# Performance work log

Measured on AMD Instinct MI355X. Metric: run time of the kernel, lower is better.

## Reference

```python
import jax, jax.numpy as jnp
import numpy as np

EPS = 1e-5
GROUPS = 8
OUT_PLANES = 256
GP = OUT_PLANES // GROUPS  # group_planes = 32


def _bn_eval(x, p, ch_axis):
    # p: [4, C] = (gamma, beta, running_mean, running_var); eval-mode batchnorm
    shape = [1] * x.ndim
    shape[ch_axis] = -1
    g, b, m, v = (p[i].reshape(shape) for i in range(4))
    return g * (x - m) * jax.lax.rsqrt(v + EPS) + b


def _make_bn(key, ch):
    k1, k2, k3, k4 = jax.random.split(key, 4)
    gamma = jax.random.uniform(k1, (ch,)) + 0.5
    beta = jax.random.normal(k2, (ch,)) * 0.1
    mean = jax.random.normal(k3, (ch,)) * 0.1
    var = jax.random.uniform(k4, (ch,)) + 0.5
    return jnp.stack([gamma, beta, mean, var])  # [4, ch]


def setup_inputs() -> dict:
    key = jax.random.key(0)
    ks = jax.random.split(key, 6)
    N, C, D, Hh, Ww = 1, 256, 16, 32, 64
    x = jax.random.normal(ks[0], (N, C, D, Hh, Ww), dtype=jnp.float32)
    # qkv 1x1 conv weight: [out_planes*2, in_planes]
    qkv_w = jax.random.normal(ks[1], (OUT_PLANES * 2, C), dtype=jnp.float32) * np.sqrt(1.0 / C)
    # relative positional table: [group_planes*2, 2*H-1]
    relative = jax.random.normal(ks[2], (GP * 2, 2 * Ww - 1), dtype=jnp.float32) * np.sqrt(1.0 / GP)
    bn_qkv = _make_bn(ks[3], OUT_PLANES * 2)
    bn_sim = _make_bn(ks[4], GROUPS * 3)
    bn_out = _make_bn(ks[5], OUT_PLANES * 2)
    return {"x": x, "qkv_w": qkv_w, "relative": relative,
            "bn_qkv": bn_qkv, "bn_sim": bn_sim, "bn_out": bn_out}


def reference(x, qkv_w, relative, bn_qkv, bn_sim, bn_out):
    N, C, D, Hh, Ww = x.shape
    G, OP, gp = GROUPS, OUT_PLANES, GP
    # width == 0: permute(0,2,3,1,4) -> [N, D, Hh, C, Ww]; attend along Ww
    xp = jnp.transpose(x, (0, 2, 3, 1, 4))
    H = Ww
    B = N * D * Hh
    xr = xp.reshape(B, C, H)
    # 1x1 conv + BN over channels
    qkv = jnp.einsum('oc,bch->boh', qkv_w, xr)
    qkv = _bn_eval(qkv, bn_qkv, 1)
    qkv = qkv.reshape(B, G, 2 * gp, H)
    q = qkv[:, :, : gp // 2]          # [B,G,gp/2,H]
    k = qkv[:, :, gp // 2: gp]        # [B,G,gp/2,H]
    v = qkv[:, :, gp:]                # [B,G,gp,H]
    # relative-position gather: emb[c,i,j] = relative[c, i-j+H-1]
    idx = jnp.arange(H)[:, None] - jnp.arange(H)[None, :] + H - 1  # [H,H]
    emb = relative[:, idx]            # [2*gp, H, H]
    q_e = emb[: gp // 2]
    k_e = emb[gp // 2: gp]
    v_e = emb[gp:]
    qr = jnp.einsum('bgci,cij->bgij', q, q_e)
    kr = jnp.einsum('bgci,cij->bgji', k, k_e)  # einsum + transpose(2,3) fused
    qk = jnp.einsum('bgci,bgcj->bgij', q, k)
    sim = jnp.concatenate([qk, qr, kr], axis=1)  # [B, 3G, H, H]
    sim = _bn_eval(sim, bn_sim, 1)
    sim = sim.reshape(B, 3, G, H, H).sum(axis=1)
    sim = jax.nn.softmax(sim, axis=3)
    sv = jnp.einsum('bgij,bgcj->bgci', sim, v)
    sve = jnp.einsum('bgij,cij->bgci', sim, v_e)
    so = jnp.concatenate([sv, sve], axis=-1).reshape(B, 2 * OP, H)
    out = _bn_eval(so, bn_out, 1)
    out = out.reshape(N, D, Hh, OP, 2, H).sum(axis=-2)
    out = jnp.transpose(out, (0, 3, 1, 2, 4))  # [N, OP, D, Hh, Ww]
    return out
```

## Files before the change

### kernel.cpp

```cpp
#include <hip/hip_runtime.h>

#define EPS 1e-5f

typedef _Float16 half4_t __attribute__((ext_vector_type(4)));
typedef _Float16 half8_t __attribute__((ext_vector_type(8)));
typedef float floatx4 __attribute__((ext_vector_type(4)));

__device__ __forceinline__ unsigned short f2hb(float f) {
  _Float16 h = (_Float16)f;
  return __builtin_bit_cast(unsigned short, h);
}
__device__ __forceinline__ float hb2f(unsigned short u) {
  return (float)__builtin_bit_cast(_Float16, u);
}
__device__ __forceinline__ unsigned int pack2(float a, float b) {
  return (unsigned int)f2hb(a) | ((unsigned int)f2hb(b) << 16);
}

#define WS_QKT 16777216
#define WS_WH 33554432
#define WS_RELTQ 33816576
#define WS_RELTK 33820672
#define WS_RELV 33824768
#define WS_BNSF 33832960
#define WS_BNOSC 33833088
#define WS_BNOSH 33835136

__global__ __launch_bounds__(256) void k_prep(const float* __restrict__ W,
                                              const float* __restrict__ rel,
                                              const float* __restrict__ bns,
                                              const float* __restrict__ bno,
                                              char* __restrict__ ws) {
  const int bid = blockIdx.x, tid = threadIdx.x;
  if (bid < 8) {
    unsigned short* Wh = (unsigned short*)(ws + WS_WH);
    const int base = bid * 16384;
#pragma unroll
    for (int u = 0; u < 16; ++u) {
      const int i = base + u * 1024 + tid * 4;
      const float4 v = *reinterpret_cast<const float4*>(&W[i]);
      uint2 p;
      p.x = pack2(v.x, v.y);
      p.y = pack2(v.z, v.w);
      *reinterpret_cast<uint2*>(&Wh[i]) = p;
    }
  } else {
    unsigned short* relTq = (unsigned short*)(ws + WS_RELTQ);
    unsigned short* relTk = (unsigned short*)(ws + WS_RELTK);
    unsigned short* relV = (unsigned short*)(ws + WS_RELV);
    float* bnsF = (float*)(ws + WS_BNSF);
    float* bnoSc = (float*)(ws + WS_BNOSC);
    float* bnoSh = (float*)(ws + WS_BNOSH);
    for (int idx = tid; idx < 2048; idx += 256) {
      const int t = idx >> 4, c = idx & 15;
      relTq[idx] = (t < 127) ? f2hb(rel[c * 127 + t]) : (unsigned short)0;
      relTk[idx] = (t < 127) ? f2hb(rel[(16 + c) * 127 + t]) : (unsigned short)0;
    }
    for (int idx = tid; idx < 4096; idx += 256) {
      const int c = idx >> 7, t = idx & 127;
      relV[idx] = (t < 127) ? f2hb(rel[(32 + c) * 127 + t]) : (unsigned short)0;
    }
    if (tid < 8) {
      const int g = tid;
      const float scA = bns[g] / sqrtf(bns[72 + g] + EPS);
      const float scB = bns[8 + g] / sqrtf(bns[72 + 8 + g] + EPS);
      const float scC = bns[16 + g] / sqrtf(bns[72 + 16 + g] + EPS);
      const float shv = (bns[24 + g] - bns[48 + g] * scA) +
                        (bns[24 + 8 + g] - bns[48 + 8 + g] * scB) +
                        (bns[24 + 16 + g] - bns[48 + 16 + g] * scC);
      bnsF[g * 4 + 0] = scA;
      bnsF[g * 4 + 1] = scB;
      bnsF[g * 4 + 2] = scC;
      bnsF[g * 4 + 3] = shv;
    }
    for (int idx = tid; idx < 512; idx += 256) {
      const float sc = bno[idx] / sqrtf(bno[1536 + idx] + EPS);
      bnoSc[idx] = sc;
      bnoSh[idx] = bno[512 + idx] - bno[1024 + idx] * sc;
    }
  }
}

__global__ __launch_bounds__(512, 4) void k_qkv(const float* __restrict__ x,
                                                const float* __restrict__ bnq,
                                                char* __restrict__ ws) {
  const unsigned short* Wh = (const unsigned short*)(ws + WS_WH);
  unsigned short* qkv_h = (unsigned short*)ws;
  unsigned short* qkT = (unsigned short*)(ws + WS_QKT);
  __shared__ __align__(16) char arena[67584];
  unsigned short* xT = (unsigned short*)arena;
  unsigned short* qk_t = (unsigned short*)arena;
  unsigned short* v_t = (unsigned short*)(arena + 33792);

  const int tid = threadIdx.x;
  const int lane = tid & 63;
  const int w = tid >> 6;
  const int l15 = lane & 15, kg = lane >> 4;
  const size_t b = blockIdx.x;
  const int n0g = (int)b * 64;

  {
    const int k = tid >> 1;
    const int nb = (tid & 1) * 32;
    const float* src = x + (size_t)k * 32768 + n0g + nb;
    unsigned short hv[32];
#pragma unroll
    for (int u = 0; u < 8; ++u) {
      const float4 v4 = *reinterpret_cast<const float4*>(src + u * 4);
      hv[u * 4 + 0] = f2hb(v4.x);
      hv[u * 4 + 1] = f2hb(v4.y);
      hv[u * 4 + 2] = f2hb(v4.z);
      hv[u * 4 + 3] = f2hb(v4.w);
    }
#pragma unroll
    for (int e = 0; e < 32; ++e) xT[(nb + e) * 280 + k] = hv[e];
  }
  __syncthreads();

  floatx4 acc[4][4] = {};
#pragma unroll
  for (int kk = 0; kk < 8; ++kk) {
    half8_t af[4], bf[4];
#pragma unroll
    for (int fm = 0; fm < 4; ++fm)
      af[fm] = *reinterpret_cast<const half8_t*>(Wh + (size_t)(w * 64 + fm * 16 + l15) * 256 +
                                                 kk * 32 + kg * 8);
#pragma unroll
    for (int fn = 0; fn < 4; ++fn)
      bf[fn] =
          *reinterpret_cast<const half8_t*>(xT + (fn * 16 + l15) * 280 + kk * 32 + kg * 8);
#pragma unroll
    for (int fm = 0; fm < 4; ++fm)
#pragma unroll
      for (int fn = 0; fn < 4; ++fn)
        acc[fm][fn] = __builtin_amdgcn_mfma_f32_16x16x32_f16(af[fm], bf[fn], acc[fm][fn], 0, 0, 0);
  }
  __syncthreads();

  const int o0 = w * 64;
#pragma unroll
  for (int fm = 0; fm < 4; ++fm) {
    float sc[4], sh[4];
#pragma unroll
    for (int reg = 0; reg < 4; ++reg) {
      const int o = o0 + fm * 16 + kg * 4 + reg;
      sc[reg] = bnq[o] / sqrtf(bnq[1536 + o] + EPS);
      sh[reg] = bnq[512 + o] - bnq[1024 + o] * sc[reg];
    }
#pragma unroll
    for (int fn = 0; fn < 4; ++fn) {
      const int h = fn * 16 + l15;
#pragma unroll
      for (int reg = 0; reg < 4; ++reg) {
        const int row = fm * 16 + kg * 4 + reg;
        const float val = fmaf(acc[fm][fn][reg], sc[reg], sh[reg]);
        if (fm < 2) {
          qk_t[w * 2112 + h * 33 + row] = f2hb(val);
        } else {
          v_t[w * 2112 + (row - 32) * 66 + h] = f2hb(val);
        }
      }
    }
  }
  __syncthreads();

  {
    const int half = tid >> 8;
    const int tt = tid & 255;
#pragma unroll
    for (int it = 0; it < 4; ++it) {
      const int g = it * 2 + half;
      {
        const int h = tt >> 2, c0 = (tt & 3) * 8;
        unsigned short tmp[8];
#pragma unroll
        for (int e = 0; e < 8; ++e) tmp[e] = qk_t[g * 2112 + h * 33 + c0 + e];
        uint4 wv;
        wv.x = (unsigned int)tmp[0] | ((unsigned int)tmp[1] << 16);
        wv.y = (unsigned int)tmp[2] | ((unsigned int)tmp[3] << 16);
        wv.z = (unsigned int)tmp[4] | ((unsigned int)tmp[5] << 16);
        wv.w = (unsigned int)tmp[6] | ((unsigned int)tmp[7] << 16);
        *reinterpret_cast<uint4*>(&qkT[((b * 8 + g) * 64 + h) * 32 + c0]) = wv;
      }
      {
        const int c = tt >> 3, h0 = (tt & 7) * 8;
        unsigned short tmp[8];
#pragma unroll
        for (int e = 0; e < 8; ++e) tmp[e] = v_t[g * 2112 + c * 66 + h0 + e];
        uint4 wv;
        wv.x = (unsigned int)tmp[0] | ((unsigned int)tmp[1] << 16);
        wv.y = (unsigned int)tmp[2] | ((unsigned int)tmp[3] << 16);
        wv.z = (unsigned int)tmp[4] | ((unsigned int)tmp[5] << 16);
        wv.w = (unsigned int)tmp[6] | ((unsigned int)tmp[7] << 16);
        *reinterpret_cast<uint4*>(&qkv_h[((b * 8 + g) * 32 + c) * 64 + h0]) = wv;
      }
    }
  }
}

#define QKS 36
#define M1S 132
#define PBS 72
#define PPS 136
#define OTS 67

__global__ __launch_bounds__(256, 4) void k_attn(const char* __restrict__ ws,
                                                 float* __restrict__ out) {
  const unsigned short* qkv_h = (const unsigned short*)ws;
  const unsigned short* qkTg = (const unsigned short*)(ws + WS_QKT);
  const unsigned short* relTq = (const unsigned short*)(ws + WS_RELTQ);
  const unsigned short* relTk = (const unsigned short*)(ws + WS_RELTK);
  const unsigned short* relV = (const unsigned short*)(ws + WS_RELV);
  const float* bnsF = (const float*)(ws + WS_BNSF);
  const float* bnoSc = (const float*)(ws + WS_BNOSC);
  const float* bnoSh = (const float*)(ws + WS_BNOSH);

  __shared__ __align__(16) char arena[38400];
  unsigned short* qkL = (unsigned short*)arena;
  unsigned short* M1 = (unsigned short*)(arena + 4608);
  unsigned short* M2 = (unsigned short*)(arena + 21504);
  unsigned short* Pb = (unsigned short*)arena;
  unsigned short* Pp = (unsigned short*)(arena + 9216);
  unsigned short* Vb = (unsigned short*)(arena + 26624);
  float* Sout = (float*)arena;

  const int tid = threadIdx.x;
  const int lane = tid & 63;
  const int wid = tid >> 6;
  const int l15 = lane & 15, kg = lane >> 4;
  const int bg = blockIdx.x;
  const int b = bg >> 3, g = bg & 7;

  {
    const uint4 qv =
        *reinterpret_cast<const uint4*>(&qkTg[(size_t)(((b << 3) + g)) * 2048 + tid * 8]);
    const int i = tid >> 2, c0 = (tid & 3) * 8;
    uint2 lo, hi;
    lo.x = qv.x; lo.y = qv.y; hi.x = qv.z; hi.y = qv.w;
    *reinterpret_cast<uint2*>(&qkL[i * QKS + c0]) = lo;
    *reinterpret_cast<uint2*>(&qkL[i * QKS + c0 + 4]) = hi;
  }
  __syncthreads();

  floatx4 qkreg[4];
  {
    half4_t brq[8], brk[8];
#pragma unroll
    for (int nt = 0; nt < 8; ++nt) {
      brq[nt] = *reinterpret_cast<const half4_t*>(&relTq[(nt * 16 + l15) * 16 + kg * 4]);
      brk[nt] = *reinterpret_cast<const half4_t*>(&relTk[(nt * 16 + l15) * 16 + kg * 4]);
    }
    const half4_t aq = *reinterpret_cast<const half4_t*>(&qkL[(wid * 16 + l15) * QKS + kg * 4]);
    const half4_t ak =
        *reinterpret_cast<const half4_t*>(&qkL[(wid * 16 + l15) * QKS + 16 + kg * 4]);
#pragma unroll
    for (int nt = 0; nt < 4; ++nt) {
      const half4_t bq =
          *reinterpret_cast<const half4_t*>(&qkL[(nt * 16 + l15) * QKS + 16 + kg * 4]);
      const floatx4 z = {};
      qkreg[nt] = __builtin_amdgcn_mfma_f32_16x16x16f16(aq, bq, z, 0, 0, 0);
    }
#pragma unroll
    for (int nt = 0; nt < 8; ++nt) {
      const floatx4 z = {};
      const floatx4 cr = __builtin_amdgcn_mfma_f32_16x16x16f16(aq, brq[nt], z, 0, 0, 0);
#pragma unroll
      for (int r = 0; r < 4; ++r)
        M1[(wid * 16 + kg * 4 + r) * M1S + nt * 16 + l15] = f2hb(cr[r]);
    }
#pragma unroll
    for (int nt = 0; nt < 8; ++nt) {
      const floatx4 z = {};
      const floatx4 cr = __builtin_amdgcn_mfma_f32_16x16x16f16(ak, brk[nt], z, 0, 0, 0);
#pragma unroll
      for (int r = 0; r < 4; ++r)
        M2[(wid * 16 + kg * 4 + r) * M1S + nt * 16 + l15] = f2hb(cr[r]);
    }
  }
  __syncthreads();

  const uint4 vld = *reinterpret_cast<const uint4*>(
      &qkv_h[(((size_t)b * 8 + g) * 32 + (tid >> 3)) * 64 + (tid & 7) * 8]);
  float sreg[4][4];
  {
    const float4 bf = *reinterpret_cast<const float4*>(&bnsF[g * 4]);
#pragma unroll
    for (int nt = 0; nt < 4; ++nt) {
      const int j = nt * 16 + l15;
#pragma unroll
      for (int r = 0; r < 4; ++r) {
        const int i = wid * 16 + kg * 4 + r;
        const int d = i - j + 63;
        const float qr = hb2f(M1[i * M1S + d]);
        const float kr = hb2f(M2[j * M1S + 126 - d]);
        sreg[nt][r] = fmaf(bf.x, qkreg[nt][r], fmaf(bf.y, qr, fmaf(bf.z, kr, bf.w)));
      }
    }
  }
  __syncthreads();

  float sm[4];
#pragma unroll
  for (int r = 0; r < 4; ++r) {
    float m = fmaxf(fmaxf(sreg[0][r], sreg[1][r]), fmaxf(sreg[2][r], sreg[3][r]));
    m = fmaxf(m, __shfl_xor(m, 1));
    m = fmaxf(m, __shfl_xor(m, 2));
    m = fmaxf(m, __shfl_xor(m, 4));
    m = fmaxf(m, __shfl_xor(m, 8));
    float s = 0.f;
#pragma unroll
    for (int nt = 0; nt < 4; ++nt) {
      sreg[nt][r] = __expf(sreg[nt][r] - m);
      s += sreg[nt][r];
    }
    s += __shfl_xor(s, 1);
    s += __shfl_xor(s, 2);
    s += __shfl_xor(s, 4);
    s += __shfl_xor(s, 8);
    sm[r] = s;
  }
#pragma unroll
  for (int r = 0; r < 4; ++r) {
    const int i = wid * 16 + kg * 4 + r;
#pragma unroll
    for (int nt = 0; nt < 4; ++nt) {
      const int j = nt * 16 + l15;
      const unsigned short pv = f2hb(sreg[nt][r]);
      Pb[i * PBS + j] = pv;
      Pp[i * PPS + i + 63 - j] = pv;
    }
#pragma unroll
    for (int e = 0; e < 4; ++e) {
      const int z = l15 * 4 + e;
      const int t = (z < i) ? z : z + 64;
      Pp[i * PPS + t] = 0;
    }
  }
  {
    *reinterpret_cast<uint4*>(&Vb[(tid >> 3) * PBS + (tid & 7) * 8]) = vld;
  }
  __syncthreads();

  floatx4 sva[2] = {}, svea[2] = {};
#pragma unroll
  for (int kk = 0; kk < 2; ++kk) {
    const half8_t pa =
        *reinterpret_cast<const half8_t*>(&Pb[(wid * 16 + l15) * PBS + kk * 32 + kg * 8]);
#pragma unroll
    for (int nt = 0; nt < 2; ++nt) {
      const half8_t vb =
          *reinterpret_cast<const half8_t*>(&Vb[(nt * 16 + l15) * PBS + kk * 32 + kg * 8]);
      sva[nt] = __builtin_amdgcn_mfma_f32_16x16x32_f16(pa, vb, sva[nt], 0, 0, 0);
    }
  }
#pragma unroll
  for (int kk = 0; kk < 4; ++kk) {
    const half8_t pp =
        *reinterpret_cast<const half8_t*>(&Pp[(wid * 16 + l15) * PPS + kk * 32 + kg * 8]);
#pragma unroll
    for (int nt = 0; nt < 2; ++nt) {
      const half8_t rb =
          *reinterpret_cast<const half8_t*>(&relV[(nt * 16 + l15) * 128 + kk * 32 + kg * 8]);
      svea[nt] = __builtin_amdgcn_mfma_f32_16x16x32_f16(pp, rb, svea[nt], 0, 0, 0);
    }
  }
  __syncthreads();

#pragma unroll
  for (int nt = 0; nt < 2; ++nt) {
    const int c = nt * 16 + l15;
    const int ch = ((g << 5) + c) * 2;
    const float2 scv = *reinterpret_cast<const float2*>(&bnoSc[ch]);
    const float2 shv = *reinterpret_cast<const float2*>(&bnoSh[ch]);
#pragma unroll
    for (int r = 0; r < 4; ++r) {
      const int i = wid * 16 + kg * 4 + r;
      const float inv = 1.0f / sm[r];
      Sout[c * OTS + i] =
          fmaf(scv.x, sva[nt][r] * inv, shv.x) + fmaf(scv.y, svea[nt][r] * inv, shv.y);
    }
  }
  __syncthreads();
  {
    const size_t outbase = (size_t)b * 64;
#pragma unroll
    for (int r = 0; r < 8; ++r) {
      const int idx = tid + r * 256;
      const int cc = idx >> 6, ii = idx & 63;
      out[(size_t)((g << 5) + cc) * 32768 + outbase + ii] = Sout[cc * OTS + ii];
    }
  }
}

extern "C" void kernel_launch(void* const* d_in, const int* in_sizes, int n_in,
                              void* d_out, int out_size, void* d_ws, size_t ws_size,
                              hipStream_t stream) {
  const float* x = (const float*)d_in[0];
  const float* qkv_w = (const float*)d_in[1];
  const float* relative = (const float*)d_in[2];
  const float* bn_qkv = (const float*)d_in[3];
  const float* bn_sim = (const float*)d_in[4];
  const float* bn_out = (const float*)d_in[5];
  float* out = (float*)d_out;
  char* ws = (char*)d_ws;

  k_prep<<<9, 256, 0, stream>>>(qkv_w, relative, bn_sim, bn_out, ws);
  k_qkv<<<512, 512, 0, stream>>>(x, bn_qkv, ws);
  k_attn<<<4096, 256, 0, stream>>>(ws, out);
}
```

Baseline: 93.90 us.

## Restructure qkv/attn epilogues: precompute BN, direct V stores, transposed MFMA outputs

```diff
diff --git a/kernel.cpp b/kernel.cpp
--- a/kernel.cpp
+++ b/kernel.cpp
@@ -25,8 +25,11 @@
 #define WS_BNSF 33832960
 #define WS_BNOSC 33833088
 #define WS_BNOSH 33835136
+#define WS_BNQSC 33837184
+#define WS_BNQSH 33839232
 
 __global__ __launch_bounds__(256) void k_prep(const float* __restrict__ W,
+                                              const float* __restrict__ bnq,
                                               const float* __restrict__ rel,
                                               const float* __restrict__ bns,
                                               const float* __restrict__ bno,
@@ -51,6 +54,8 @@
     float* bnsF = (float*)(ws + WS_BNSF);
     float* bnoSc = (float*)(ws + WS_BNOSC);
     float* bnoSh = (float*)(ws + WS_BNOSH);
+    float* bnqSc = (float*)(ws + WS_BNQSC);
+    float* bnqSh = (float*)(ws + WS_BNQSH);
     for (int idx = tid; idx < 2048; idx += 256) {
       const int t = idx >> 4, c = idx & 15;
       relTq[idx] = (t < 127) ? f2hb(rel[c * 127 + t]) : (unsigned short)0;
@@ -77,20 +82,23 @@
       const float sc = bno[idx] / sqrtf(bno[1536 + idx] + EPS);
       bnoSc[idx] = sc;
       bnoSh[idx] = bno[512 + idx] - bno[1024 + idx] * sc;
-    }
-  }
-}
-
-__global__ __launch_bounds__(512, 4) void k_qkv(const float* __restrict__ x,
-                                                const float* __restrict__ bnq,
+      const float qc = bnq[idx] / sqrtf(bnq[1536 + idx] + EPS);
+      bnqSc[idx] = qc;
+      bnqSh[idx] = bnq[512 + idx] - bnq[1024 + idx] * qc;
+    }
+  }
+}
+
+__global__ __launch_bounds__(512, 8) void k_qkv(const float* __restrict__ x,
                                                 char* __restrict__ ws) {
   const unsigned short* Wh = (const unsigned short*)(ws + WS_WH);
+  const float* bnqSc = (const float*)(ws + WS_BNQSC);
+  const float* bnqSh = (const float*)(ws + WS_BNQSH);
   unsigned short* qkv_h = (unsigned short*)ws;
   unsigned short* qkT = (unsigned short*)(ws + WS_QKT);
-  __shared__ __align__(16) char arena[67584];
+  __shared__ __align__(16) char arena[36864];
   unsigned short* xT = (unsigned short*)arena;
   unsigned short* qk_t = (unsigned short*)arena;
-  unsigned short* v_t = (unsigned short*)(arena + 33792);
 
   const int tid = threadIdx.x;
   const int lane = tid & 63;
@@ -127,8 +135,7 @@
                                                  kk * 32 + kg * 8);
 #pragma unroll
     for (int fn = 0; fn < 4; ++fn)
-      bf[fn] =
-          *reinterpret_cast<const half8_t*>(xT + (fn * 16 + l15) * 280 + kk * 32 + kg * 8);
+      bf[fn] = *reinterpret_cast<const half8_t*>(xT + (fn * 16 + l15) * 280 + kk * 32 + kg * 8);
 #pragma unroll
     for (int fm = 0; fm < 4; ++fm)
 #pragma unroll
@@ -140,69 +147,52 @@
   const int o0 = w * 64;
 #pragma unroll
   for (int fm = 0; fm < 4; ++fm) {
-    float sc[4], sh[4];
-#pragma unroll
-    for (int reg = 0; reg < 4; ++reg) {
-      const int o = o0 + fm * 16 + kg * 4 + reg;
-      sc[reg] = bnq[o] / sqrtf(bnq[1536 + o] + EPS);
-      sh[reg] = bnq[512 + o] - bnq[1024 + o] * sc[reg];
-    }
+    const float4 sc4 = *reinterpret_cast<const float4*>(&bnqSc[o0 + fm * 16 + kg * 4]);
+    const float4 sh4 = *reinterpret_cast<const float4*>(&bnqSh[o0 + fm * 16 + kg * 4]);
 #pragma unroll
     for (int fn = 0; fn < 4; ++fn) {
       const int h = fn * 16 + l15;
-#pragma unroll
-      for (int reg = 0; reg < 4; ++reg) {
-        const int row = fm * 16 + kg * 4 + reg;
-        const float val = fmaf(acc[fm][fn][reg], sc[reg], sh[reg]);
-        if (fm < 2) {
-          qk_t[w * 2112 + h * 33 + row] = f2hb(val);
-        } else {
-          v_t[w * 2112 + (row - 32) * 66 + h] = f2hb(val);
-        }
+      const float v0 = fmaf(acc[fm][fn][0], sc4.x, sh4.x);
+      const float v1 = fmaf(acc[fm][fn][1], sc4.y, sh4.y);
+      const float v2 = fmaf(acc[fm][fn][2], sc4.z, sh4.z);
+      const float v3 = fmaf(acc[fm][fn][3], sc4.w, sh4.w);
+      if (fm < 2) {
+        uint2 p;
+        p.x = pack2(v0, v1);
+        p.y = pack2(v2, v3);
+        *reinterpret_cast<uint2*>(&qk_t[w * 2304 + h * 36 + fm * 16 + kg * 4]) = p;
+      } else {
+        const int cb = (fm - 2) * 16 + kg * 4;
+        unsigned short* dst = &qkv_h[((b * 8 + w) * 32 + cb) * 64 + h];
+        dst[0] = f2hb(v0);
+        dst[64] = f2hb(v1);
+        dst[128] = f2hb(v2);
+        dst[192] = f2hb(v3);
       }
     }
   }
   __syncthreads();
-
-  {
-    const int half = tid >> 8;
-    const int tt = tid & 255;
-#pragma unroll
-    for (int it = 0; it < 4; ++it) {
-      const int g = it * 2 + half;
-      {
-        const int h = tt >> 2, c0 = (tt & 3) * 8;
-        unsigned short tmp[8];
-#pragma unroll
-        for (int e = 0; e < 8; ++e) tmp[e] = qk_t[g * 2112 + h * 33 + c0 + e];
-        uint4 wv;
-        wv.x = (unsigned int)tmp[0] | ((unsigned int)tmp[1] << 16);
-        wv.y = (unsigned int)tmp[2] | ((unsigned int)tmp[3] << 16);
-        wv.z = (unsigned int)tmp[4] | ((unsigned int)tmp[5] << 16);
-        wv.w = (unsigned int)tmp[6] | ((unsigned int)tmp[7] << 16);
-        *reinterpret_cast<uint4*>(&qkT[((b * 8 + g) * 64 + h) * 32 + c0]) = wv;
-      }
-      {
-        const int c = tt >> 3, h0 = (tt & 7) * 8;
-        unsigned short tmp[8];
-#pragma unroll
-        for (int e = 0; e < 8; ++e) tmp[e] = v_t[g * 2112 + c * 66 + h0 + e];
-        uint4 wv;
-        wv.x = (unsigned int)tmp[0] | ((unsigned int)tmp[1] << 16);
-        wv.y = (unsigned int)tmp[2] | ((unsigned int)tmp[3] << 16);
-        wv.z = (unsigned int)tmp[4] | ((unsigned int)tmp[5] << 16);
-        wv.w = (unsigned int)tmp[6] | ((unsigned int)tmp[7] << 16);
-        *reinterpret_cast<uint4*>(&qkv_h[((b * 8 + g) * 32 + c) * 64 + h0]) = wv;
-      }
-    }
+#pragma unroll
+  for (int it = 0; it < 4; ++it) {
+    const int idx = it * 512 + tid;
+    const int g2 = idx >> 8, e = idx & 255;
+    const int h = e >> 2, c0 = (e & 3) * 8;
+    const unsigned short* srcp = &qk_t[g2 * 2304 + h * 36 + c0];
+    const uint2 a = *reinterpret_cast<const uint2*>(srcp);
+    const uint2 b2 = *reinterpret_cast<const uint2*>(srcp + 4);
+    uint4 wv;
+    wv.x = a.x;
+    wv.y = a.y;
+    wv.z = b2.x;
+    wv.w = b2.y;
+    *reinterpret_cast<uint4*>(&qkT[((b * 8 + g2) * 64 + h) * 32 + c0]) = wv;
   }
 }
 
 #define QKS 36
-#define M1S 132
+#define MTS 68
 #define PBS 72
 #define PPS 136
-#define OTS 67
 
 __global__ __launch_bounds__(256, 4) void k_attn(const char* __restrict__ ws,
                                                  float* __restrict__ out) {
@@ -215,14 +205,14 @@
   const float* bnoSc = (const float*)(ws + WS_BNOSC);
   const float* bnoSh = (const float*)(ws + WS_BNOSH);
 
-  __shared__ __align__(16) char arena[38400];
+  __shared__ __align__(16) char arena[39424];
   unsigned short* qkL = (unsigned short*)arena;
-  unsigned short* M1 = (unsigned short*)(arena + 4608);
-  unsigned short* M2 = (unsigned short*)(arena + 21504);
+  unsigned short* M1T = (unsigned short*)(arena + 4608);
+  unsigned short* M2T = (unsigned short*)(arena + 22016);
   unsigned short* Pb = (unsigned short*)arena;
   unsigned short* Pp = (unsigned short*)(arena + 9216);
   unsigned short* Vb = (unsigned short*)(arena + 26624);
-  float* Sout = (float*)arena;
+  float* rowsumL = (float*)(arena + 31232);
 
   const int tid = threadIdx.x;
   const int lane = tid & 63;
@@ -236,7 +226,10 @@
         *reinterpret_cast<const uint4*>(&qkTg[(size_t)(((b << 3) + g)) * 2048 + tid * 8]);
     const int i = tid >> 2, c0 = (tid & 3) * 8;
     uint2 lo, hi;
-    lo.x = qv.x; lo.y = qv.y; hi.x = qv.z; hi.y = qv.w;
+    lo.x = qv.x;
+    lo.y = qv.y;
+    hi.x = qv.z;
+    hi.y = qv.w;
     *reinterpret_cast<uint2*>(&qkL[i * QKS + c0]) = lo;
     *reinterpret_cast<uint2*>(&qkL[i * QKS + c0 + 4]) = hi;
   }
@@ -260,21 +253,24 @@
       const floatx4 z = {};
       qkreg[nt] = __builtin_amdgcn_mfma_f32_16x16x16f16(aq, bq, z, 0, 0, 0);
     }
+    const int mcol = wid * 16 + kg * 4;
 #pragma unroll
     for (int nt = 0; nt < 8; ++nt) {
       const floatx4 z = {};
       const floatx4 cr = __builtin_amdgcn_mfma_f32_16x16x16f16(aq, brq[nt], z, 0, 0, 0);
-#pragma unroll
-      for (int r = 0; r < 4; ++r)
-        M1[(wid * 16 + kg * 4 + r) * M1S + nt * 16 + l15] = f2hb(cr[r]);
+      uint2 p;
+      p.x = pack2(cr[0], cr[1]);
+      p.y = pack2(cr[2], cr[3]);
+      *reinterpret_cast<uint2*>(&M1T[(nt * 16 + l15) * MTS + mcol]) = p;
     }
 #pragma unroll
     for (int nt = 0; nt < 8; ++nt) {
       const floatx4 z = {};
       const floatx4 cr = __builtin_amdgcn_mfma_f32_16x16x16f16(ak, brk[nt], z, 0, 0, 0);
-#pragma unroll
-      for (int r = 0; r < 4; ++r)
-        M2[(wid * 16 + kg * 4 + r) * M1S + nt * 16 + l15] = f2hb(cr[r]);
+      uint2 p;
+      p.x = pack2(cr[0], cr[1]);
+      p.y = pack2(cr[2], cr[3]);
+      *reinterpret_cast<uint2*>(&M2T[(nt * 16 + l15) * MTS + mcol]) = p;
     }
   }
   __syncthreads();
@@ -291,8 +287,8 @@
       for (int r = 0; r < 4; ++r) {
         const int i = wid * 16 + kg * 4 + r;
         const int d = i - j + 63;
-        const float qr = hb2f(M1[i * M1S + d]);
-        const float kr = hb2f(M2[j * M1S + 126 - d]);
+        const float qr = hb2f(M1T[d * MTS + i]);
+        const float kr = hb2f(M2T[(126 - d) * MTS + j]);
         sreg[nt][r] = fmaf(bf.x, qkreg[nt][r], fmaf(bf.y, qr, fmaf(bf.z, kr, bf.w)));
       }
     }
@@ -322,6 +318,24 @@
 #pragma unroll
   for (int r = 0; r < 4; ++r) {
     const int i = wid * 16 + kg * 4 + r;
+    const int z0 = l15 * 4;
+    if (z0 + 3 < i) {
+      uint2 zz;
+      zz.x = 0u;
+      zz.y = 0u;
+      *reinterpret_cast<uint2*>(&Pp[i * PPS + z0]) = zz;
+    } else if (z0 >= i) {
+      uint2 zz;
+      zz.x = 0u;
+      zz.y = 0u;
+      *reinterpret_cast<uint2*>(&Pp[i * PPS + z0 + 64]) = zz;
+    } else {
+#pragma unroll
+      for (int e = 0; e < 4; ++e) {
+        const int z = z0 + e;
+        Pp[i * PPS + (z < i ? z : z + 64)] = 0;
+      }
+    }
 #pragma unroll
     for (int nt = 0; nt < 4; ++nt) {
       const int j = nt * 16 + l15;
@@ -329,12 +343,7 @@
       Pb[i * PBS + j] = pv;
       Pp[i * PPS + i + 63 - j] = pv;
     }
-#pragma unroll
-    for (int e = 0; e < 4; ++e) {
-      const int z = l15 * 4 + e;
-      const int t = (z < i) ? z : z + 64;
-      Pp[i * PPS + t] = 0;
-    }
+    if (l15 == 0) rowsumL[i] = sm[r];
   }
   {
     *reinterpret_cast<uint4*>(&Vb[(tid >> 3) * PBS + (tid & 7) * 8]) = vld;
@@ -344,50 +353,40 @@
   floatx4 sva[2] = {}, svea[2] = {};
 #pragma unroll
   for (int kk = 0; kk < 2; ++kk) {
-    const half8_t pa =
+    const half8_t pbf =
         *reinterpret_cast<const half8_t*>(&Pb[(wid * 16 + l15) * PBS + kk * 32 + kg * 8]);
 #pragma unroll
-    for (int nt = 0; nt < 2; ++nt) {
+    for (int cf = 0; cf < 2; ++cf) {
       const half8_t vb =
-          *reinterpret_cast<const half8_t*>(&Vb[(nt * 16 + l15) * PBS + kk * 32 + kg * 8]);
-      sva[nt] = __builtin_amdgcn_mfma_f32_16x16x32_f16(pa, vb, sva[nt], 0, 0, 0);
+          *reinterpret_cast<const half8_t*>(&Vb[(cf * 16 + l15) * PBS + kk * 32 + kg * 8]);
+      sva[cf] = __builtin_amdgcn_mfma_f32_16x16x32_f16(vb, pbf, sva[cf], 0, 0, 0);
     }
   }
 #pragma unroll
   for (int kk = 0; kk < 4; ++kk) {
-    const half8_t pp =
+    const half8_t ppf =
         *reinterpret_cast<const half8_t*>(&Pp[(wid * 16 + l15) * PPS + kk * 32 + kg * 8]);
 #pragma unroll
-    for (int nt = 0; nt < 2; ++nt) {
+    for (int cf = 0; cf < 2; ++cf) {
       const half8_t rb =
-          *reinterpret_cast<const half8_t*>(&relV[(nt * 16 + l15) * 128 + kk * 32 + kg * 8]);
-      svea[nt] = __builtin_amdgcn_mfma_f32_16x16x32_f16(pp, rb, svea[nt], 0, 0, 0);
-    }
-  }
-  __syncthreads();
-
-#pragma unroll
-  for (int nt = 0; nt < 2; ++nt) {
-    const int c = nt * 16 + l15;
-    const int ch = ((g << 5) + c) * 2;
-    const float2 scv = *reinterpret_cast<const float2*>(&bnoSc[ch]);
-    const float2 shv = *reinterpret_cast<const float2*>(&bnoSh[ch]);
-#pragma unroll
-    for (int r = 0; r < 4; ++r) {
-      const int i = wid * 16 + kg * 4 + r;
-      const float inv = 1.0f / sm[r];
-      Sout[c * OTS + i] =
-          fmaf(scv.x, sva[nt][r] * inv, shv.x) + fmaf(scv.y, svea[nt][r] * inv, shv.y);
-    }
-  }
-  __syncthreads();
-  {
-    const size_t outbase = (size_t)b * 64;
-#pragma unroll
-    for (int r = 0; r < 8; ++r) {
-      const int idx = tid + r * 256;
-      const int cc = idx >> 6, ii = idx & 63;
-      out[(size_t)((g << 5) + cc) * 32768 + outbase + ii] = Sout[cc * OTS + ii];
+          *reinterpret_cast<const half8_t*>(&relV[(cf * 16 + l15) * 128 + kk * 32 + kg * 8]);
+      svea[cf] = __builtin_amdgcn_mfma_f32_16x16x32_f16(rb, ppf, svea[cf], 0, 0, 0);
+    }
+  }
+  {
+    const int i = wid * 16 + l15;
+    const float inv = 1.0f / rowsumL[i];
+#pragma unroll
+    for (int cf = 0; cf < 2; ++cf) {
+#pragma unroll
+      for (int reg = 0; reg < 4; ++reg) {
+        const int c = cf * 16 + kg * 4 + reg;
+        const int ch = ((g << 5) + c) * 2;
+        const float2 scv = *reinterpret_cast<const float2*>(&bnoSc[ch]);
+        const float2 shv = *reinterpret_cast<const float2*>(&bnoSh[ch]);
+        out[(size_t)((g << 5) + c) * 32768 + (size_t)b * 64 + i] =
+            fmaf(scv.x, sva[cf][reg] * inv, shv.x) + fmaf(scv.y, svea[cf][reg] * inv, shv.y);
+      }
     }
   }
 }
@@ -404,7 +403,7 @@
   float* out = (float*)d_out;
   char* ws = (char*)d_ws;
 
-  k_prep<<<9, 256, 0, stream>>>(qkv_w, relative, bn_sim, bn_out, ws);
-  k_qkv<<<512, 512, 0, stream>>>(x, bn_qkv, ws);
+  k_prep<<<9, 256, 0, stream>>>(qkv_w, bn_qkv, relative, bn_sim, bn_out, ws);
+  k_qkv<<<512, 512, 0, stream>>>(x, ws);
   k_attn<<<4096, 256, 0, stream>>>(ws, out);
 }
```

Result: slower. 186.8 us (+98.9%).
